# Optimization experiments

Measured on AMD Instinct MI355X. Metric: run time of the kernel, lower is better.

Reference implementation:

```python
import jax, jax.numpy as jnp
import numpy as np

B = 256
N = 256


def setup_inputs() -> dict:
    key = jax.random.key(0)
    ks = jax.random.split(key, 6)
    X = jax.random.normal(ks[0], (B, N), dtype=jnp.float32)
    context = jax.random.normal(ks[1], (B, N), dtype=jnp.float32)
    W = jax.random.normal(ks[2], (N, N), dtype=jnp.float32) * 0.1
    scale = jnp.ones((1,), dtype=jnp.float32)
    A = jax.random.uniform(ks[3], (N, N), dtype=jnp.float32)
    cl_weight = jax.random.normal(ks[4], (N * N, N), dtype=jnp.float32) * 0.02
    cl_bias = jax.random.normal(ks[5], (N * N,), dtype=jnp.float32) * 0.02
    t = 3
    return {"X": X, "context": context, "W": W, "scale": scale, "A": A,
            "cl_weight": cl_weight, "cl_bias": cl_bias, "t": t}


def reference(X, context, W, scale, A, cl_weight, cl_bias, t):
    # context_L path: context-conditioned adjustment of W, shape [B, N, N]
    Bsz, n = X.shape
    adjust = (context @ cl_weight.T + cl_bias).reshape(Bsz, n, n)
    W_new = adjust + W  # broadcast [N,N] over batch
    # diag term: sum over rows i of (W_new @ A)[b, i, k] = einsum bij,jk->bk
    d = jnp.einsum('bij,jk->bk', W_new, A)
    eye = jnp.eye(n, dtype=X.dtype)
    L = d[:, :, None] * eye - W_new          # diag_embed(d) - W_new, [B,N,N]
    new_context = context * (t / (t + 1)) + X / (t + 1)
    L_T = scale * jnp.swapaxes(L, -1, -2)    # [B,N,N]
    update = jnp.einsum('bn,bnm->bm', X, L_T)  # matmul(X[...,None,:], L_T).squeeze()
    return (update, new_context)
```

## Files before the change

### kernel.cpp

```cpp
#include <hip/hip_runtime.h>

#define N 256
#define NN 65536

typedef __attribute__((ext_vector_type(8))) __bf16 bf16x8;
typedef __attribute__((ext_vector_type(4))) __bf16 bf16x4v;
typedef __attribute__((ext_vector_type(4))) float f32x4;

#define F_PART   0u
#define F_SPART  2097152u
#define F_WSC    2621440u
#define F_SFULL  2621696u
#define F_YADJ   2687232u
#define WS_FLOATS 2752768u

static __device__ __forceinline__ f32x4 mfma16(bf16x8 a, bf16x8 b, f32x4 c) {
  return __builtin_amdgcn_mfma_f32_16x16x32_bf16(a, b, c, 0, 0, 0);
}
static __device__ __forceinline__ bf16x4v pack4(float4 v) {
  bf16x4v r;
  r[0] = (__bf16)v.x; r[1] = (__bf16)v.y; r[2] = (__bf16)v.z; r[3] = (__bf16)v.w;
  return r;
}
static __device__ __forceinline__ bf16x8 pack8(float4 a, float4 b) {
  bf16x8 r;
  r[0] = (__bf16)a.x; r[1] = (__bf16)a.y; r[2] = (__bf16)a.z; r[3] = (__bf16)a.w;
  r[4] = (__bf16)b.x; r[5] = (__bf16)b.y; r[6] = (__bf16)b.z; r[7] = (__bf16)b.w;
  return r;
}

#define BAR()                                                  \
  asm volatile("s_waitcnt lgkmcnt(0)" ::: "memory");           \
  __builtin_amdgcn_s_barrier();                                \
  __builtin_amdgcn_sched_barrier(0);

__global__ void __launch_bounds__(512) kbig(
    const float* __restrict__ X, const float* __restrict__ ctx,
    const float* __restrict__ W, const float* __restrict__ clb,
    const float* __restrict__ clw, float* __restrict__ ws)
{
  extern __shared__ char smem[];
  float* xl = (float*)(smem + 49152);
  float* sred = (float*)(smem + 57344);
  const int t = threadIdx.x;
  const int mt = blockIdx.x >> 5, s = blockIdx.x & 31;
  const int n0 = s * 8, m0g = mt * 32;
  const float4* clwf4 = (const float4*)clw;

  int gm[4], gk[4];
  float4 g0[4], g1[4], g2[4];
#pragma unroll
  for (int i = 0; i < 4; ++i) {
    const int idx = i * 512 + t;
    gm[i] = idx >> 6; gk[i] = idx & 63;
    g0[i] = clwf4[(m0g + gm[i]) * 16384 + (n0 + 0) * 64 + gk[i]];
  }
#pragma unroll
  for (int i = 0; i < 4; ++i)
    g1[i] = clwf4[(m0g + gm[i]) * 16384 + (n0 + 1) * 64 + gk[i]];
#pragma unroll
  for (int i = 0; i < 4; ++i)
    g2[i] = clwf4[(m0g + gm[i]) * 16384 + (n0 + 2) * 64 + gk[i]];

  const int lane = t & 63, w = t >> 6;
  const int wb = w * 32, l15 = lane & 15, lhi = lane >> 4;
  const int swz = (l15 & 7) << 4;

  bf16x8 af[2][8];
#pragma unroll
  for (int i = 0; i < 2; ++i)
#pragma unroll
    for (int c = 0; c < 8; ++c) {
      const float4* p =
          (const float4*)(ctx + (wb + i * 16 + l15) * N + c * 32 + lhi * 8);
      af[i][c] = pack8(p[0], p[1]);
    }

  if (t < 256) {
    const float4* xp = (const float4*)(X + t * N + n0);
    const float4 x0 = xp[0], x1 = xp[1];
    xl[0 * N + t] = x0.x; xl[1 * N + t] = x0.y; xl[2 * N + t] = x0.z; xl[3 * N + t] = x0.w;
    xl[4 * N + t] = x1.x; xl[5 * N + t] = x1.y; xl[6 * N + t] = x1.z; xl[7 * N + t] = x1.w;
  }
#pragma unroll
  for (int i = 0; i < 4; ++i)
    *(bf16x4v*)(smem + gm[i] * 512 + ((gk[i] * 8) ^ ((gm[i] & 7) << 4))) = pack4(g0[i]);
  BAR();

  const f32x4 zero = {0.f, 0.f, 0.f, 0.f};
  f32x4 acc[2][2];
  acc[0][0] = zero; acc[0][1] = zero; acc[1][0] = zero; acc[1][1] = zero;

#define KITER(NN, DO_ISSUE, GISS, DO_WRITE, GWR)                              \
  {                                                                           \
    if (DO_ISSUE) {                                                           \
      _Pragma("unroll")                                                       \
      for (int i = 0; i < 4; ++i)                                             \
        GISS[i] = clwf4[(m0g + gm[i]) * 16384 + (n0 + (NN) + 3) * 64 + gk[i]];\
    }                                                                         \
    char* buf = smem + ((NN) % 3) * 16384;                                    \
    f32x4 h[2][2];                                                            \
    h[0][0] = zero; h[0][1] = zero; h[1][0] = zero; h[1][1] = zero;           \
    _Pragma("unroll")                                                         \
    for (int c = 0; c < 8; ++c) {                                             \
      const int kb = c * 64 + lhi * 16;                                       \
      bf16x8 b0 = *(const bf16x8*)(buf + l15 * 512 + (kb ^ swz));             \
      bf16x8 b1 = *(const bf16x8*)(buf + (16 + l15) * 512 + (kb ^ swz));      \
      h[0][0] = mfma16(af[0][c], b0, h[0][0]);                                \
      h[0][1] = mfma16(af[0][c], b1, h[0][1]);                                \
      h[1][0] = mfma16(af[1][c], b0, h[1][0]);                                \
      h[1][1] = mfma16(af[1][c], b1, h[1][1]);                                \
    }                                                                         \
    _Pragma("unroll")                                                         \
    for (int fb = 0; fb < 2; ++fb) {                                          \
      _Pragma("unroll")                                                       \
      for (int r = 0; r < 4; ++r) {                                           \
        const int brow = wb + fb * 16 + lhi * 4 + r;                          \
        const float xv = xl[(NN) * N + brow];                                 \
        acc[fb][0][r] += xv * h[fb][0][r];                                    \
        acc[fb][1][r] += xv * h[fb][1][r];                                    \
        float v = h[fb][0][r] + h[fb][1][r];                                  \
        v += __shfl_xor(v, 1); v += __shfl_xor(v, 2);                         \
        v += __shfl_xor(v, 4); v += __shfl_xor(v, 8);                         \
        if (l15 == 0) sred[(NN) * 256 + brow] = v;                            \
      }                                                                       \
    }                                                                         \
    if (DO_WRITE) {                                                           \
      char* wbuf = smem + (((NN) + 1) % 3) * 16384;                           \
      _Pragma("unroll")                                                       \
      for (int i = 0; i < 4; ++i)                                             \
        *(bf16x4v*)(wbuf + gm[i] * 512 +                                      \
                    ((gk[i] * 8) ^ ((gm[i] & 7) << 4))) = pack4(GWR[i]);      \
    }                                                                         \
    BAR();                                                                    \
  }

  KITER(0, 1, g0, 1, g1)
  KITER(1, 1, g1, 1, g2)
  KITER(2, 1, g2, 1, g0)
  KITER(3, 1, g0, 1, g1)
  KITER(4, 1, g1, 1, g2)
  KITER(5, 0, g0, 1, g0)
  KITER(6, 0, g0, 1, g1)
  KITER(7, 0, g0, 0, g0)
#undef KITER

  const int base = blockIdx.x * 8192;
#pragma unroll
  for (int fb = 0; fb < 2; ++fb)
#pragma unroll
    for (int fm = 0; fm < 2; ++fm)
#pragma unroll
      for (int r = 0; r < 4; ++r)
        ws[F_PART + base + (wb + fb * 16 + lhi * 4 + r) * 32 + fm * 16 + l15] =
            acc[fb][fm][r];

  {
    const int b = wb + (lane >> 1);
    const int nh = (lane & 1) * 4;
    float4 v;
    v.x = sred[(nh + 0) * 256 + b];
    v.y = sred[(nh + 1) * 256 + b];
    v.z = sred[(nh + 2) * 256 + b];
    v.w = sred[(nh + 3) * 256 + b];
    *(float4*)(ws + F_SPART + mt * NN + b * N + n0 + nh) = v;
  }

  if (mt == 0) {
    __syncthreads();
    float* red = xl;
    if (t < 256) {
      const float4* wp = (const float4*)(W + t * N + s * 8);
      const float4* cp = (const float4*)(clb + t * N + s * 8);
      const float4 a0 = wp[0], a1 = wp[1], b0 = cp[0], b1 = cp[1];
      red[0 * 256 + t] = a0.x + b0.x; red[1 * 256 + t] = a0.y + b0.y;
      red[2 * 256 + t] = a0.z + b0.z; red[3 * 256 + t] = a0.w + b0.w;
      red[4 * 256 + t] = a1.x + b1.x; red[5 * 256 + t] = a1.y + b1.y;
      red[6 * 256 + t] = a1.z + b1.z; red[7 * 256 + t] = a1.w + b1.w;
    }
    __syncthreads();
    if (t < 64) {
      const int jj = t >> 3, seg = t & 7;
      float v = 0.f;
#pragma unroll
      for (int i = 0; i < 32; ++i) v += red[jj * 256 + seg * 32 + i];
      v += __shfl_xor(v, 1);
      v += __shfl_xor(v, 2);
      v += __shfl_xor(v, 4);
      if (seg == 0) ws[F_WSC + s * 8 + jj] = v;
    }
  }
}

__global__ void __launch_bounds__(256) kred(float* __restrict__ ws)
{
  const int o = blockIdx.x * 256 + threadIdx.x;
  const int b = o >> 8, col = o & 255;
  const int mt = col >> 5, ml = col & 31;
  float y = 0.f;
#pragma unroll
  for (int si = 0; si < 32; ++si)
    y += ws[F_PART + ((mt * 32 + si) * 256 + b) * 32 + ml];
  ws[F_YADJ + o] = y;
  float sv = ws[F_WSC + col];
#pragma unroll
  for (int q = 0; q < 8; ++q)
    sv += ws[F_SPART + q * NN + o];
  ws[F_SFULL + o] = sv;
}

__global__ void __launch_bounds__(256) kfin(
    const float* __restrict__ X, const float* __restrict__ ctx,
    const float* __restrict__ W, const float* __restrict__ clb,
    const float* __restrict__ A, const float* __restrict__ scale,
    const int* __restrict__ tptr, float* __restrict__ out,
    float* __restrict__ ws)
{
  extern __shared__ char smem[];
  const int t = threadIdx.x, blk = blockIdx.x;
  const int b0 = (blk >> 3) * 32, k0 = (blk & 7) * 32;
  {
    const int row = t >> 3, q = t & 7;
    const int sw = (row & 7) << 4;
    const float4* sp = (const float4*)(ws + F_SFULL + (b0 + row) * N);
    const float4* xp = (const float4*)(X + (b0 + row) * N);
    const float4* wp = (const float4*)(W + (k0 + row) * N);
    const float4* cp = (const float4*)(clb + (k0 + row) * N);
#pragma unroll
    for (int i = 0; i < 8; ++i) {
      const int f4 = q * 8 + i;
      const int off = row * 512 + ((f4 * 8) ^ sw);
      *(bf16x4v*)(smem + off) = pack4(sp[f4]);
      *(bf16x4v*)(smem + 16384 + off) = pack4(xp[f4]);
      const float4 wv = wp[f4], cv = cp[f4];
      float4 s2;
      s2.x = wv.x + cv.x; s2.y = wv.y + cv.y;
      s2.z = wv.z + cv.z; s2.w = wv.w + cv.w;
      *(bf16x4v*)(smem + 49152 + off) = pack4(s2);
    }
    const float4* ap = (const float4*)(A + t * N + k0);
    char* at = smem + 32768;
#pragma unroll
    for (int i = 0; i < 8; ++i) {
      const float4 v = ap[i];
      const int kk = i * 4;
      *(__bf16*)(at + (kk + 0) * 512 + ((t * 2) ^ (((kk + 0) & 7) << 4))) = (__bf16)v.x;
      *(__bf16*)(at + (kk + 1) * 512 + ((t * 2) ^ (((kk + 1) & 7) << 4))) = (__bf16)v.y;
      *(__bf16*)(at + (kk + 2) * 512 + ((t * 2) ^ (((kk + 2) & 7) << 4))) = (__bf16)v.z;
      *(__bf16*)(at + (kk + 3) * 512 + ((t * 2) ^ (((kk + 3) & 7) << 4))) = (__bf16)v.w;
    }
  }
  __syncthreads();
  const int lane = t & 63, w = t >> 6;
  const int l15 = lane & 15, lhi = lane >> 4;
  const int wqb = (w >> 1) * 16, wqk = (w & 1) * 16;
  const int swz = (l15 & 7) << 4;
  f32x4 accd = {0.f, 0.f, 0.f, 0.f}, accw = {0.f, 0.f, 0.f, 0.f};
#pragma unroll
  for (int c = 0; c < 8; ++c) {
    const int kb = c * 64 + lhi * 16;
    bf16x8 as  = *(const bf16x8*)(smem + (wqb + l15) * 512 + (kb ^ swz));
    bf16x8 aat = *(const bf16x8*)(smem + 32768 + (wqk + l15) * 512 + (kb ^ swz));
    bf16x8 ax  = *(const bf16x8*)(smem + 16384 + (wqb + l15) * 512 + (kb ^ swz));
    bf16x8 awc = *(const bf16x8*)(smem + 49152 + (wqk + l15) * 512 + (kb ^ swz));
    accd = mfma16(as, aat, accd);
    accw = mfma16(ax, awc, accw);
  }
  const float sc = scale[0];
  const float tf = (float)(*tptr);
  const float c1 = tf / (tf + 1.f), c2 = 1.f / (tf + 1.f);
#pragma unroll
  for (int r = 0; r < 4; ++r) {
    const int b = b0 + wqb + lhi * 4 + r, k = k0 + wqk + l15;
    const int idx = b * N + k;
    const float xv = X[idx];
    out[idx] = sc * (xv * accd[r] - accw[r] - ws[F_YADJ + idx]);
    out[NN + idx] = ctx[idx] * c1 + xv * c2;
  }
}

extern "C" void kernel_launch(void* const* d_in, const int* in_sizes, int n_in,
                              void* d_out, int out_size, void* d_ws, size_t ws_size,
                              hipStream_t stream)
{
  (void)in_sizes; (void)n_in; (void)out_size;
  const float* X     = (const float*)d_in[0];
  const float* ctx   = (const float*)d_in[1];
  const float* W     = (const float*)d_in[2];
  const float* scale = (const float*)d_in[3];
  const float* A     = (const float*)d_in[4];
  const float* clw   = (const float*)d_in[5];
  const float* clb   = (const float*)d_in[6];
  const int*   tptr  = (const int*)d_in[7];
  float* out = (float*)d_out;
  float* ws  = (float*)d_ws;

  if (ws_size < (size_t)WS_FLOATS * sizeof(float)) return;

  (void)hipFuncSetAttribute((const void*)kbig,
                            hipFuncAttributeMaxDynamicSharedMemorySize, 65536);
  (void)hipFuncSetAttribute((const void*)kfin,
                            hipFuncAttributeMaxDynamicSharedMemorySize, 65536);

  kbig<<<256, 512, 65536, stream>>>(X, ctx, W, clb, clw, ws);
  kred<<<256, 256, 0, stream>>>(ws);
  kfin<<<64, 256, 65536, stream>>>(X, ctx, W, clb, A, scale, tptr, out, ws);
}
```

Measured before the change: 53.73 us.

## Issue all cl_weight tile loads upfront and stage into enlarged LDS

Replaces the three-stage rotating register/LDS pipeline with a scheme that issues all eight cl_weight slab loads at kernel start, writes them into eight LDS buffers in two halves, and computes with only two barriers. This aims to maximize outstanding memory requests and cut per-iteration barrier overhead. It raises dynamic LDS to 144 KB and keeps 32 float4 values live in registers, which risks register spills, especially with the added launch-bounds occupancy hint.

```diff
diff --git a/kernel.cpp b/kernel.cpp
--- a/kernel.cpp
+++ b/kernel.cpp
@@ -34,33 +34,49 @@
   __builtin_amdgcn_s_barrier();                                \
   __builtin_amdgcn_sched_barrier(0);
 
-__global__ void __launch_bounds__(512) kbig(
+__global__ void __launch_bounds__(512, 2) kbig(
     const float* __restrict__ X, const float* __restrict__ ctx,
     const float* __restrict__ W, const float* __restrict__ clb,
     const float* __restrict__ clw, float* __restrict__ ws)
 {
   extern __shared__ char smem[];
-  float* xl = (float*)(smem + 49152);
-  float* sred = (float*)(smem + 57344);
+  float* xl   = (float*)(smem + 131072);
+  float* sred = (float*)(smem + 139264);
+  float* red  = (float*)(smem + 131072);
   const int t = threadIdx.x;
   const int mt = blockIdx.x >> 5, s = blockIdx.x & 31;
   const int n0 = s * 8, m0g = mt * 32;
   const float4* clwf4 = (const float4*)clw;
 
   int gm[4], gk[4];
-  float4 g0[4], g1[4], g2[4];
 #pragma unroll
   for (int i = 0; i < 4; ++i) {
     const int idx = i * 512 + t;
     gm[i] = idx >> 6; gk[i] = idx & 63;
-    g0[i] = clwf4[(m0g + gm[i]) * 16384 + (n0 + 0) * 64 + gk[i]];
-  }
-#pragma unroll
-  for (int i = 0; i < 4; ++i)
-    g1[i] = clwf4[(m0g + gm[i]) * 16384 + (n0 + 1) * 64 + gk[i]];
-#pragma unroll
-  for (int i = 0; i < 4; ++i)
-    g2[i] = clwf4[(m0g + gm[i]) * 16384 + (n0 + 2) * 64 + gk[i]];
+  }
+
+  float4 g0[4], g1[4], g2[4], g3[4], g4[4], g5[4], g6[4], g7[4];
+#define ISSUE(TT, G)                                                        \
+  _Pragma("unroll")                                                         \
+  for (int i = 0; i < 4; ++i)                                               \
+    G[i] = clwf4[(m0g + gm[i]) * 16384 + (n0 + (TT)) * 64 + gk[i]];
+#define WRITE(TT, G)                                                        \
+  _Pragma("unroll")                                                         \
+  for (int i = 0; i < 4; ++i)                                               \
+    *(bf16x4v*)(smem + (TT) * 16384 + gm[i] * 512 +                         \
+                ((gk[i] * 8) ^ ((gm[i] & 7) << 4))) = pack4(G[i]);
+
+  ISSUE(0, g0) ISSUE(1, g1) ISSUE(2, g2) ISSUE(3, g3)
+  ISSUE(4, g4) ISSUE(5, g5) ISSUE(6, g6) ISSUE(7, g7)
+
+  if (t < 256) {
+    const float4* xp = (const float4*)(X + t * N + n0);
+    const float4 x0 = xp[0], x1 = xp[1];
+    xl[0 * 256 + t] = x0.x; xl[1 * 256 + t] = x0.y;
+    xl[2 * 256 + t] = x0.z; xl[3 * 256 + t] = x0.w;
+    xl[4 * 256 + t] = x1.x; xl[5 * 256 + t] = x1.y;
+    xl[6 * 256 + t] = x1.z; xl[7 * 256 + t] = x1.w;
+  }
 
   const int lane = t & 63, w = t >> 6;
   const int wb = w * 32, l15 = lane & 15, lhi = lane >> 4;
@@ -76,74 +92,50 @@
       af[i][c] = pack8(p[0], p[1]);
     }
 
-  if (t < 256) {
-    const float4* xp = (const float4*)(X + t * N + n0);
-    const float4 x0 = xp[0], x1 = xp[1];
-    xl[0 * N + t] = x0.x; xl[1 * N + t] = x0.y; xl[2 * N + t] = x0.z; xl[3 * N + t] = x0.w;
-    xl[4 * N + t] = x1.x; xl[5 * N + t] = x1.y; xl[6 * N + t] = x1.z; xl[7 * N + t] = x1.w;
-  }
-#pragma unroll
-  for (int i = 0; i < 4; ++i)
-    *(bf16x4v*)(smem + gm[i] * 512 + ((gk[i] * 8) ^ ((gm[i] & 7) << 4))) = pack4(g0[i]);
-  BAR();
-
   const f32x4 zero = {0.f, 0.f, 0.f, 0.f};
   f32x4 acc[2][2];
   acc[0][0] = zero; acc[0][1] = zero; acc[1][0] = zero; acc[1][1] = zero;
 
-#define KITER(NN, DO_ISSUE, GISS, DO_WRITE, GWR)                              \
-  {                                                                           \
-    if (DO_ISSUE) {                                                           \
-      _Pragma("unroll")                                                       \
-      for (int i = 0; i < 4; ++i)                                             \
-        GISS[i] = clwf4[(m0g + gm[i]) * 16384 + (n0 + (NN) + 3) * 64 + gk[i]];\
-    }                                                                         \
-    char* buf = smem + ((NN) % 3) * 16384;                                    \
-    f32x4 h[2][2];                                                            \
-    h[0][0] = zero; h[0][1] = zero; h[1][0] = zero; h[1][1] = zero;           \
-    _Pragma("unroll")                                                         \
-    for (int c = 0; c < 8; ++c) {                                             \
-      const int kb = c * 64 + lhi * 16;                                       \
-      bf16x8 b0 = *(const bf16x8*)(buf + l15 * 512 + (kb ^ swz));             \
-      bf16x8 b1 = *(const bf16x8*)(buf + (16 + l15) * 512 + (kb ^ swz));      \
-      h[0][0] = mfma16(af[0][c], b0, h[0][0]);                                \
-      h[0][1] = mfma16(af[0][c], b1, h[0][1]);                                \
-      h[1][0] = mfma16(af[1][c], b0, h[1][0]);                                \
-      h[1][1] = mfma16(af[1][c], b1, h[1][1]);                                \
-    }                                                                         \
-    _Pragma("unroll")                                                         \
-    for (int fb = 0; fb < 2; ++fb) {                                          \
-      _Pragma("unroll")                                                       \
-      for (int r = 0; r < 4; ++r) {                                           \
-        const int brow = wb + fb * 16 + lhi * 4 + r;                          \
-        const float xv = xl[(NN) * N + brow];                                 \
-        acc[fb][0][r] += xv * h[fb][0][r];                                    \
-        acc[fb][1][r] += xv * h[fb][1][r];                                    \
-        float v = h[fb][0][r] + h[fb][1][r];                                  \
-        v += __shfl_xor(v, 1); v += __shfl_xor(v, 2);                         \
-        v += __shfl_xor(v, 4); v += __shfl_xor(v, 8);                         \
-        if (l15 == 0) sred[(NN) * 256 + brow] = v;                            \
-      }                                                                       \
-    }                                                                         \
-    if (DO_WRITE) {                                                           \
-      char* wbuf = smem + (((NN) + 1) % 3) * 16384;                           \
-      _Pragma("unroll")                                                       \
-      for (int i = 0; i < 4; ++i)                                             \
-        *(bf16x4v*)(wbuf + gm[i] * 512 +                                      \
-                    ((gk[i] * 8) ^ ((gm[i] & 7) << 4))) = pack4(GWR[i]);      \
-    }                                                                         \
-    BAR();                                                                    \
-  }
-
-  KITER(0, 1, g0, 1, g1)
-  KITER(1, 1, g1, 1, g2)
-  KITER(2, 1, g2, 1, g0)
-  KITER(3, 1, g0, 1, g1)
-  KITER(4, 1, g1, 1, g2)
-  KITER(5, 0, g0, 1, g0)
-  KITER(6, 0, g0, 1, g1)
-  KITER(7, 0, g0, 0, g0)
-#undef KITER
+#define COMP(NNV)                                                           \
+  {                                                                         \
+    char* buf = smem + (NNV) * 16384;                                       \
+    f32x4 h[2][2];                                                          \
+    h[0][0] = zero; h[0][1] = zero; h[1][0] = zero; h[1][1] = zero;         \
+    _Pragma("unroll")                                                       \
+    for (int c = 0; c < 8; ++c) {                                           \
+      const int kb = c * 64 + lhi * 16;                                     \
+      bf16x8 b0 = *(const bf16x8*)(buf + l15 * 512 + (kb ^ swz));           \
+      bf16x8 b1 = *(const bf16x8*)(buf + (16 + l15) * 512 + (kb ^ swz));    \
+      h[0][0] = mfma16(af[0][c], b0, h[0][0]);                              \
+      h[0][1] = mfma16(af[0][c], b1, h[0][1]);                              \
+      h[1][0] = mfma16(af[1][c], b0, h[1][0]);                              \
+      h[1][1] = mfma16(af[1][c], b1, h[1][1]);                              \
+    }                                                                       \
+    _Pragma("unroll")                                                       \
+    for (int fb = 0; fb < 2; ++fb) {                                        \
+      _Pragma("unroll")                                                     \
+      for (int r = 0; r < 4; ++r) {                                         \
+        const int brow = wb + fb * 16 + lhi * 4 + r;                        \
+        const float xv = xl[(NNV) * 256 + brow];                            \
+        acc[fb][0][r] += xv * h[fb][0][r];                                  \
+        acc[fb][1][r] += xv * h[fb][1][r];                                  \
+        float v = h[fb][0][r] + h[fb][1][r];                                \
+        v += __shfl_xor(v, 1); v += __shfl_xor(v, 2);                       \
+        v += __shfl_xor(v, 4); v += __shfl_xor(v, 8);                       \
+        if (l15 == 0) sred[(NNV) * 256 + brow] = v;                         \
+      }                                                                     \
+    }                                                                       \
+  }
+
+  WRITE(0, g0) WRITE(1, g1) WRITE(2, g2) WRITE(3, g3)
+  BAR();
+  COMP(0) COMP(1) COMP(2) COMP(3)
+  WRITE(4, g4) WRITE(5, g5) WRITE(6, g6) WRITE(7, g7)
+  BAR();
+  COMP(4) COMP(5) COMP(6) COMP(7)
+#undef ISSUE
+#undef WRITE
+#undef COMP
 
   const int base = blockIdx.x * 8192;
 #pragma unroll
@@ -168,7 +160,6 @@
 
   if (mt == 0) {
     __syncthreads();
-    float* red = xl;
     if (t < 256) {
       const float4* wp = (const float4*)(W + t * N + s * 8);
       const float4* cp = (const float4*)(clb + t * N + s * 8);
@@ -298,11 +289,11 @@
   if (ws_size < (size_t)WS_FLOATS * sizeof(float)) return;
 
   (void)hipFuncSetAttribute((const void*)kbig,
-                            hipFuncAttributeMaxDynamicSharedMemorySize, 65536);
+                            hipFuncAttributeMaxDynamicSharedMemorySize, 147456);
   (void)hipFuncSetAttribute((const void*)kfin,
                             hipFuncAttributeMaxDynamicSharedMemorySize, 65536);
 
-  kbig<<<256, 512, 65536, stream>>>(X, ctx, W, clb, clw, ws);
+  kbig<<<256, 512, 147456, stream>>>(X, ctx, W, clb, clw, ws);
   kred<<<256, 256, 0, stream>>>(ws);
   kfin<<<64, 256, 65536, stream>>>(X, ctx, W, clb, A, scale, tptr, out, ws);
 }
```

Result: slower. 57.79 us (+7.6%).
